# Kernel optimization log

Measured on AMD Instinct MI355X. Metric: run time of the kernel, lower is better.

## Reference

```python
import jax, jax.numpy as jnp
import numpy as np

E = 128       # estimators
R = 65536     # regions per estimator
S = 100000    # update samples


def setup_inputs() -> dict:
    key = jax.random.key(0)
    k1, k2, k3, k4, k5 = jax.random.split(key, 5)
    a = jax.random.uniform(k1, (E, R), dtype=jnp.float32) + 0.1
    b = jax.random.uniform(k2, (E, R), dtype=jnp.float32) + 0.1
    samples_regions = jax.random.randint(k3, (S, E), 0, R, dtype=jnp.int32)
    da = jax.random.uniform(k4, (S,), dtype=jnp.float32)
    db = jax.random.uniform(k5, (S,), dtype=jnp.float32)
    return {"a": a, "b": b, "samples_regions": samples_regions, "da": da, "db": db}


def reference(a, b, samples_regions, da, db):
    # Original: lax.scan over samples, each step vmapping over estimators and
    # doing beliefs.a.at[region].add(da). Addition is commutative, so the whole
    # scan is a single batched scatter-add into the [E, R] tables.
    est = jnp.arange(a.shape[0], dtype=samples_regions.dtype)[None, :]  # [1, E]
    new_a = a.at[est, samples_regions].add(da[:, None])  # indices broadcast to [S, E]
    new_b = b.at[est, samples_regions].add(db[:, None])
    return jnp.stack([new_a, new_b])  # [2, E, R]
```

## Files before the change

kernel.cpp:

```cpp
#include <hip/hip_runtime.h>

#define NE 128
#define NR 65536
#define NS 100000
#define NSP 100096
#define NG8 (NS / 8)
#define NG8_MAIN 12288

#define CHUNK4 32768
#define CHUNK 16384

#define FXS16   2048.0f
#define FXI16   4.8828125e-4f
#define FXQ16(vv) ((unsigned)__builtin_fmaf((vv), FXS16, 0.5f))

typedef float vfloat4 __attribute__((ext_vector_type(4)));
typedef unsigned short u16x8 __attribute__((ext_vector_type(8)));

__global__ __launch_bounds__(256) void EnsembleBeliefs_transpose16(
    const int* __restrict__ in,
    unsigned short* __restrict__ outT,
    const float* __restrict__ da,
    const float* __restrict__ db,
    unsigned* __restrict__ qv)
{
    __shared__ int tile[64 * 128];
    const int t  = threadIdx.x;
    const int s0 = blockIdx.x * 64;

    {
        const int idx = blockIdx.x * 256 + t;
        if (idx < NS / 4) {
            const float4 va = ((const float4*)da)[idx];
            const float4 vb = ((const float4*)db)[idx];
            uint4 q;
            q.x = FXQ16(va.x) | (FXQ16(vb.x) << 16);
            q.y = FXQ16(va.y) | (FXQ16(vb.y) << 16);
            q.z = FXQ16(va.z) | (FXQ16(vb.z) << 16);
            q.w = FXQ16(va.w) | (FXQ16(vb.w) << 16);
            ((uint4*)qv)[idx] = q;
        }
    }

#pragma unroll
    for (int k = 0; k < 8; ++k) {
        const int idx = k * 256 + t;
        const int sl  = idx >> 5;
        const int c4  = idx & 31;
        const int s   = s0 + sl;
        if (s < NS) {
            const int4 v = *(const int4*)(in + (size_t)s * NE + 4 * c4);
            const int swz = c4 ^ (sl & 31) ^ ((sl >> 3) & 7);
            *(int4*)&tile[sl * 128 + 4 * swz] = v;
        }
    }
    __syncthreads();

#pragma unroll
    for (int k = 0; k < 4; ++k) {
        const int u  = k * 256 + t;
        const int c3 = u & 7;
        const int e  = u >> 3;
        const int ec = e >> 2;
        const int ew = e & 3;
        unsigned w[4];
#pragma unroll
        for (int p = 0; p < 4; ++p) {
            const int r0 = 8 * c3 + 2 * p;
            const int r1 = r0 + 1;
            const unsigned lo = (unsigned)tile[r0 * 128 + 4 * (ec ^ (r0 & 31) ^ ((r0 >> 3) & 7)) + ew] & 0xffffu;
            const unsigned hi = (unsigned)tile[r1 * 128 + 4 * (ec ^ (r1 & 31) ^ ((r1 >> 3) & 7)) + ew] << 16;
            w[p] = lo | hi;
        }
        *(uint4*)(outT + (size_t)e * NSP + s0 + 8 * c3) = make_uint4(w[0], w[1], w[2], w[3]);
    }
}

#define H5_AT(rr, qq)                                                          \
    { const int _rl = (int)(rr) - base;                                        \
      if ((unsigned)_rl < (unsigned)CHUNK4) atomicAdd(&h[_rl], (qq)); }

#define H5_GROUP(rv, q0, q1)                                                   \
    H5_AT(rv[0], (q0).x) H5_AT(rv[1], (q0).y) H5_AT(rv[2], (q0).z) H5_AT(rv[3], (q0).w) \
    H5_AT(rv[4], (q1).x) H5_AT(rv[5], (q1).y) H5_AT(rv[6], (q1).z) H5_AT(rv[7], (q1).w)

__global__ __launch_bounds__(1024) void EnsembleBeliefs_hist5(
    const unsigned short* __restrict__ regT,
    const unsigned* __restrict__ qv,
    const float* __restrict__ a,
    const float* __restrict__ b,
    float* __restrict__ out)
{
    extern __shared__ unsigned h[];
    const int e    = blockIdx.x;
    const int base = blockIdx.y << 15;
    const int tid  = threadIdx.x;

    const u16x8* reg8 = (const u16x8*)(regT + (size_t)e * NSP);
    const uint4* q4   = (const uint4*)qv;

    u16x8 rA  = reg8[tid];
    uint4 qA0 = q4[2 * tid];
    uint4 qA1 = q4[2 * tid + 1];
    u16x8 rB  = reg8[tid + 1024];
    uint4 qB0 = q4[2 * (tid + 1024)];
    uint4 qB1 = q4[2 * (tid + 1024) + 1];

    uint4* h4 = (uint4*)h;
    for (int j = tid; j < CHUNK4 / 4; j += 1024) h4[j] = make_uint4(0u, 0u, 0u, 0u);
    __syncthreads();

    for (int k = 2; k < 12; ++k) {
        const int ip = tid + (k << 10);
        const u16x8 rN  = reg8[ip];
        const uint4 qN0 = q4[2 * ip];
        const uint4 qN1 = q4[2 * ip + 1];
        __builtin_amdgcn_sched_barrier(0);
        H5_GROUP(rA, qA0, qA1)
        rA = rB; qA0 = qB0; qA1 = qB1;
        rB = rN; qB0 = qN0; qB1 = qN1;
    }
    H5_GROUP(rA, qA0, qA1)
    H5_GROUP(rB, qB0, qB1)

    if (tid < NG8 - NG8_MAIN) {
        const int ip = NG8_MAIN + tid;
        const u16x8 r  = reg8[ip];
        const uint4 t0 = q4[2 * ip];
        const uint4 t1 = q4[2 * ip + 1];
        H5_GROUP(r, t0, t1)
    }
    __syncthreads();

    const size_t off = ((size_t)e << 16) + (size_t)base;
    const vfloat4* srcA = (const vfloat4*)(a + off);
    const vfloat4* srcB = (const vfloat4*)(b + off);
    vfloat4* dstA = (vfloat4*)(out + off);
    vfloat4* dstB = (vfloat4*)(out + (((size_t)NE << 16)) + off);
    for (int j = tid; j < CHUNK4 / 4; j += 1024) {
        const uint4 x = h4[j];
        const vfloat4 sa = __builtin_nontemporal_load(srcA + j);
        const vfloat4 sb = __builtin_nontemporal_load(srcB + j);
        vfloat4 oa, ob;
        oa.x = __builtin_fmaf((float)(x.x & 0xffffu), FXI16, sa.x);
        ob.x = __builtin_fmaf((float)(x.x >> 16),     FXI16, sb.x);
        oa.y = __builtin_fmaf((float)(x.y & 0xffffu), FXI16, sa.y);
        ob.y = __builtin_fmaf((float)(x.y >> 16),     FXI16, sb.y);
        oa.z = __builtin_fmaf((float)(x.z & 0xffffu), FXI16, sa.z);
        ob.z = __builtin_fmaf((float)(x.z >> 16),     FXI16, sb.z);
        oa.w = __builtin_fmaf((float)(x.w & 0xffffu), FXI16, sa.w);
        ob.w = __builtin_fmaf((float)(x.w >> 16),     FXI16, sb.w);
        __builtin_nontemporal_store(oa, dstA + j);
        __builtin_nontemporal_store(ob, dstB + j);
    }
}

#define H5S_AT(rr, qq)                                                         \
    { const int _rl = (int)(rr) - base;                                        \
      if ((unsigned)_rl < (unsigned)CHUNK) atomicAdd(&hs[_rl], (qq)); }

__global__ __launch_bounds__(1024) void EnsembleBeliefs_hist5s(
    const unsigned short* __restrict__ regT,
    const unsigned* __restrict__ qv,
    const float* __restrict__ a,
    const float* __restrict__ b,
    float* __restrict__ out)
{
    __shared__ unsigned hs[CHUNK];
    const int e    = blockIdx.x;
    const int base = blockIdx.y << 14;
    const int tid  = threadIdx.x;

    uint4* h4 = (uint4*)hs;
    for (int j = tid; j < CHUNK / 4; j += 1024) h4[j] = make_uint4(0u, 0u, 0u, 0u);
    __syncthreads();

    const u16x8* reg8 = (const u16x8*)(regT + (size_t)e * NSP);
    const uint4* q4   = (const uint4*)qv;
    for (int i = tid; i < NG8; i += 1024) {
        const u16x8 r  = reg8[i];
        const uint4 t0 = q4[2 * i];
        const uint4 t1 = q4[2 * i + 1];
        H5S_AT(r[0], t0.x) H5S_AT(r[1], t0.y) H5S_AT(r[2], t0.z) H5S_AT(r[3], t0.w)
        H5S_AT(r[4], t1.x) H5S_AT(r[5], t1.y) H5S_AT(r[6], t1.z) H5S_AT(r[7], t1.w)
    }
    __syncthreads();

    const size_t off = ((size_t)e << 16) + (size_t)base;
    const vfloat4* srcA = (const vfloat4*)(a + off);
    const vfloat4* srcB = (const vfloat4*)(b + off);
    vfloat4* dstA = (vfloat4*)(out + off);
    vfloat4* dstB = (vfloat4*)(out + (((size_t)NE << 16)) + off);
    for (int j = tid; j < CHUNK / 4; j += 1024) {
        const uint4 x = h4[j];
        const vfloat4 sa = __builtin_nontemporal_load(srcA + j);
        const vfloat4 sb = __builtin_nontemporal_load(srcB + j);
        vfloat4 oa, ob;
        oa.x = __builtin_fmaf((float)(x.x & 0xffffu), FXI16, sa.x);
        ob.x = __builtin_fmaf((float)(x.x >> 16),     FXI16, sb.x);
        oa.y = __builtin_fmaf((float)(x.y & 0xffffu), FXI16, sa.y);
        ob.y = __builtin_fmaf((float)(x.y >> 16),     FXI16, sb.y);
        oa.z = __builtin_fmaf((float)(x.z & 0xffffu), FXI16, sa.z);
        ob.z = __builtin_fmaf((float)(x.z >> 16),     FXI16, sb.z);
        oa.w = __builtin_fmaf((float)(x.w & 0xffffu), FXI16, sa.w);
        ob.w = __builtin_fmaf((float)(x.w >> 16),     FXI16, sb.w);
        __builtin_nontemporal_store(oa, dstA + j);
        __builtin_nontemporal_store(ob, dstB + j);
    }
}

__global__ __launch_bounds__(256) void EnsembleBeliefs_scatter(
    const int* __restrict__ regions,
    const float* __restrict__ da,
    const float* __restrict__ db,
    float* __restrict__ out)
{
    const int idx = blockIdx.x * 256 + threadIdx.x;
    const int s = idx >> 7;
    const int e = idx & (NE - 1);
    const int region = regions[idx];
    const size_t off = ((size_t)e << 16) + (size_t)region;
    atomicAdd(out + off, da[s]);
    atomicAdd(out + ((size_t)NE << 16) + off, db[s]);
}

extern "C" void kernel_launch(void* const* d_in, const int* in_sizes, int n_in,
                              void* d_out, int out_size, void* d_ws, size_t ws_size,
                              hipStream_t stream) {
    const float* a       = (const float*)d_in[0];
    const float* b       = (const float*)d_in[1];
    const int*   regions = (const int*)  d_in[2];
    const float* da      = (const float*)d_in[3];
    const float* db      = (const float*)d_in[4];
    float* out = (float*)d_out;

    const size_t regT16_bytes = (size_t)NE * NSP * sizeof(unsigned short);
    const size_t qv_bytes     = (size_t)NS * sizeof(unsigned);

    if (ws_size >= regT16_bytes + qv_bytes) {
        unsigned short* regT16 = (unsigned short*)d_ws;
        unsigned*       qv     = (unsigned*)((char*)d_ws + regT16_bytes);

        EnsembleBeliefs_transpose16<<<(NS + 63) / 64, 256, 0, stream>>>(
            regions, regT16, da, db, qv);

        static int big_lds = -1;
        if (big_lds < 0) {
            big_lds = (hipFuncSetAttribute(
                           reinterpret_cast<const void*>(EnsembleBeliefs_hist5),
                           hipFuncAttributeMaxDynamicSharedMemorySize,
                           CHUNK4 * (int)sizeof(unsigned)) == hipSuccess) ? 1 : 0;
        }

        if (big_lds) {
            dim3 hgrid(NE, 2);
            EnsembleBeliefs_hist5<<<hgrid, 1024, CHUNK4 * sizeof(unsigned), stream>>>(
                regT16, qv, a, b, out);
        } else {
            dim3 hgrid(NE, 4);
            EnsembleBeliefs_hist5s<<<hgrid, 1024, 0, stream>>>(regT16, qv, a, b, out);
        }
    } else {
        const size_t tbl_elems = (size_t)NE * NR;
        (void)hipMemcpyAsync(out, a, tbl_elems * sizeof(float), hipMemcpyDeviceToDevice, stream);
        (void)hipMemcpyAsync(out + tbl_elems, b, tbl_elems * sizeof(float), hipMemcpyDeviceToDevice, stream);
        EnsembleBeliefs_scatter<<<(NS * NE) / 256, 256, 0, stream>>>(regions, da, db, out);
    }
}
```

Baseline: 173.7 us.

## Use 64KB static LDS histogram with four region chunks and single-stage prefetch

Replaces the 128KB dynamic-LDS histogram kernel (2 chunks per estimator) with a 64KB static-LDS variant over 4 chunks, keeping the software-pipelined loads at one stage of prefetch instead of two. Smaller LDS per block may let two blocks share a CU and raises the block count, but each block now rescans all samples for a quarter of the regions, doubling the total index and weight reads. It also drops the hipFuncSetAttribute path and the fallback kernel.

```diff
diff --git a/kernel.cpp b/kernel.cpp
--- a/kernel.cpp
+++ b/kernel.cpp
@@ -7,7 +7,6 @@
 #define NG8 (NS / 8)
 #define NG8_MAIN 12288
 
-#define CHUNK4 32768
 #define CHUNK 16384
 
 #define FXS16   2048.0f
@@ -76,113 +75,54 @@
     }
 }
 
-#define H5_AT(rr, qq)                                                          \
+#define H6_AT(rr, qq)                                                          \
     { const int _rl = (int)(rr) - base;                                        \
-      if ((unsigned)_rl < (unsigned)CHUNK4) atomicAdd(&h[_rl], (qq)); }
+      if ((unsigned)_rl < (unsigned)CHUNK) atomicAdd(&h[_rl], (qq)); }
 
-#define H5_GROUP(rv, q0, q1)                                                   \
-    H5_AT(rv[0], (q0).x) H5_AT(rv[1], (q0).y) H5_AT(rv[2], (q0).z) H5_AT(rv[3], (q0).w) \
-    H5_AT(rv[4], (q1).x) H5_AT(rv[5], (q1).y) H5_AT(rv[6], (q1).z) H5_AT(rv[7], (q1).w)
+#define H6_GROUP(rv, q0, q1)                                                   \
+    H6_AT(rv[0], (q0).x) H6_AT(rv[1], (q0).y) H6_AT(rv[2], (q0).z) H6_AT(rv[3], (q0).w) \
+    H6_AT(rv[4], (q1).x) H6_AT(rv[5], (q1).y) H6_AT(rv[6], (q1).z) H6_AT(rv[7], (q1).w)
 
-__global__ __launch_bounds__(1024) void EnsembleBeliefs_hist5(
+__global__ __launch_bounds__(1024) void EnsembleBeliefs_hist6(
     const unsigned short* __restrict__ regT,
     const unsigned* __restrict__ qv,
     const float* __restrict__ a,
     const float* __restrict__ b,
     float* __restrict__ out)
 {
-    extern __shared__ unsigned h[];
+    __shared__ unsigned h[CHUNK];
     const int e    = blockIdx.x;
-    const int base = blockIdx.y << 15;
+    const int base = blockIdx.y << 14;
     const int tid  = threadIdx.x;
 
     const u16x8* reg8 = (const u16x8*)(regT + (size_t)e * NSP);
     const uint4* q4   = (const uint4*)qv;
 
-    u16x8 rA  = reg8[tid];
-    uint4 qA0 = q4[2 * tid];
-    uint4 qA1 = q4[2 * tid + 1];
-    u16x8 rB  = reg8[tid + 1024];
-    uint4 qB0 = q4[2 * (tid + 1024)];
-    uint4 qB1 = q4[2 * (tid + 1024) + 1];
+    u16x8 rC  = reg8[tid];
+    uint4 qC0 = q4[2 * tid];
+    uint4 qC1 = q4[2 * tid + 1];
 
     uint4* h4 = (uint4*)h;
-    for (int j = tid; j < CHUNK4 / 4; j += 1024) h4[j] = make_uint4(0u, 0u, 0u, 0u);
+    for (int j = tid; j < CHUNK / 4; j += 1024) h4[j] = make_uint4(0u, 0u, 0u, 0u);
     __syncthreads();
 
-    for (int k = 2; k < 12; ++k) {
+    for (int k = 1; k < 12; ++k) {
         const int ip = tid + (k << 10);
         const u16x8 rN  = reg8[ip];
         const uint4 qN0 = q4[2 * ip];
         const uint4 qN1 = q4[2 * ip + 1];
         __builtin_amdgcn_sched_barrier(0);
-        H5_GROUP(rA, qA0, qA1)
-        rA = rB; qA0 = qB0; qA1 = qB1;
-        rB = rN; qB0 = qN0; qB1 = qN1;
+        H6_GROUP(rC, qC0, qC1)
+        rC = rN; qC0 = qN0; qC1 = qN1;
     }
-    H5_GROUP(rA, qA0, qA1)
-    H5_GROUP(rB, qB0, qB1)
+    H6_GROUP(rC, qC0, qC1)
 
     if (tid < NG8 - NG8_MAIN) {
         const int ip = NG8_MAIN + tid;
         const u16x8 r  = reg8[ip];
         const uint4 t0 = q4[2 * ip];
         const uint4 t1 = q4[2 * ip + 1];
-        H5_GROUP(r, t0, t1)
-    }
-    __syncthreads();
-
-    const size_t off = ((size_t)e << 16) + (size_t)base;
-    const vfloat4* srcA = (const vfloat4*)(a + off);
-    const vfloat4* srcB = (const vfloat4*)(b + off);
-    vfloat4* dstA = (vfloat4*)(out + off);
-    vfloat4* dstB = (vfloat4*)(out + (((size_t)NE << 16)) + off);
-    for (int j = tid; j < CHUNK4 / 4; j += 1024) {
-        const uint4 x = h4[j];
-        const vfloat4 sa = __builtin_nontemporal_load(srcA + j);
-        const vfloat4 sb = __builtin_nontemporal_load(srcB + j);
-        vfloat4 oa, ob;
-        oa.x = __builtin_fmaf((float)(x.x & 0xffffu), FXI16, sa.x);
-        ob.x = __builtin_fmaf((float)(x.x >> 16),     FXI16, sb.x);
-        oa.y = __builtin_fmaf((float)(x.y & 0xffffu), FXI16, sa.y);
-        ob.y = __builtin_fmaf((float)(x.y >> 16),     FXI16, sb.y);
-        oa.z = __builtin_fmaf((float)(x.z & 0xffffu), FXI16, sa.z);
-        ob.z = __builtin_fmaf((float)(x.z >> 16),     FXI16, sb.z);
-        oa.w = __builtin_fmaf((float)(x.w & 0xffffu), FXI16, sa.w);
-        ob.w = __builtin_fmaf((float)(x.w >> 16),     FXI16, sb.w);
-        __builtin_nontemporal_store(oa, dstA + j);
-        __builtin_nontemporal_store(ob, dstB + j);
-    }
-}
-
-#define H5S_AT(rr, qq)                                                         \
-    { const int _rl = (int)(rr) - base;                                        \
-      if ((unsigned)_rl < (unsigned)CHUNK) atomicAdd(&hs[_rl], (qq)); }
-
-__global__ __launch_bounds__(1024) void EnsembleBeliefs_hist5s(
-    const unsigned short* __restrict__ regT,
-    const unsigned* __restrict__ qv,
-    const float* __restrict__ a,
-    const float* __restrict__ b,
-    float* __restrict__ out)
-{
-    __shared__ unsigned hs[CHUNK];
-    const int e    = blockIdx.x;
-    const int base = blockIdx.y << 14;
-    const int tid  = threadIdx.x;
-
-    uint4* h4 = (uint4*)hs;
-    for (int j = tid; j < CHUNK / 4; j += 1024) h4[j] = make_uint4(0u, 0u, 0u, 0u);
-    __syncthreads();
-
-    const u16x8* reg8 = (const u16x8*)(regT + (size_t)e * NSP);
-    const uint4* q4   = (const uint4*)qv;
-    for (int i = tid; i < NG8; i += 1024) {
-        const u16x8 r  = reg8[i];
-        const uint4 t0 = q4[2 * i];
-        const uint4 t1 = q4[2 * i + 1];
-        H5S_AT(r[0], t0.x) H5S_AT(r[1], t0.y) H5S_AT(r[2], t0.z) H5S_AT(r[3], t0.w)
-        H5S_AT(r[4], t1.x) H5S_AT(r[5], t1.y) H5S_AT(r[6], t1.z) H5S_AT(r[7], t1.w)
+        H6_GROUP(r, t0, t1)
     }
     __syncthreads();
 
@@ -244,22 +184,8 @@
         EnsembleBeliefs_transpose16<<<(NS + 63) / 64, 256, 0, stream>>>(
             regions, regT16, da, db, qv);
 
-        static int big_lds = -1;
-        if (big_lds < 0) {
-            big_lds = (hipFuncSetAttribute(
-                           reinterpret_cast<const void*>(EnsembleBeliefs_hist5),
-                           hipFuncAttributeMaxDynamicSharedMemorySize,
-                           CHUNK4 * (int)sizeof(unsigned)) == hipSuccess) ? 1 : 0;
-        }
-
-        if (big_lds) {
-            dim3 hgrid(NE, 2);
-            EnsembleBeliefs_hist5<<<hgrid, 1024, CHUNK4 * sizeof(unsigned), stream>>>(
-                regT16, qv, a, b, out);
-        } else {
-            dim3 hgrid(NE, 4);
-            EnsembleBeliefs_hist5s<<<hgrid, 1024, 0, stream>>>(regT16, qv, a, b, out);
-        }
+        dim3 hgrid(NE, 4);
+        EnsembleBeliefs_hist6<<<hgrid, 1024, 0, stream>>>(regT16, qv, a, b, out);
     } else {
         const size_t tbl_elems = (size_t)NE * NR;
         (void)hipMemcpyAsync(out, a, tbl_elems * sizeof(float), hipMemcpyDeviceToDevice, stream);
```

Result: no change. 174.9 us (+0.7%).
